# Optimization experiments

Measured on AMD Instinct MI355X. Metric: run time of the kernel, lower is better.

Reference implementation:

```python
import jax, jax.numpy as jnp
import numpy as np
from jax import lax

B, T, IN, H = 256, 128, 512, 1024
C = IN + H  # concat size


def setup_inputs() -> dict:
    key = jax.random.key(0)
    ks = jax.random.split(key, 32)
    d = {}
    names = ["F", "O", "CY", "CI", "CP", "CN", "IY", "II", "IP", "IN"]
    for i, n in enumerate(names):
        d["W" + n] = jax.random.normal(ks[i], (C, H), jnp.float32) * (2.0 / C) ** 0.5
        d["b" + n] = jax.random.uniform(ks[10 + i], (H,), jnp.float32)
    d["wA"] = jax.random.normal(ks[20], (H, H), jnp.float32) * (2.0 / H) ** 0.5
    for j, n in enumerate(["bAY", "bAI", "bAP", "bAN"]):
        d[n] = jax.random.uniform(ks[21 + j], (H,), jnp.float32)
    for j, n in enumerate(["factorY", "factorI", "factorP", "factorN"]):
        d[n] = jax.random.normal(ks[25 + j], (B, T, IN), jnp.float32)
    return d


def reference(factorY, factorI, factorP, factorN,
              WF, bF, WO, bO, WCY, bCY, WCI, bCI, WCP, bCP, WCN, bCN,
              WIY, bIY, WII, bII, WIP, bIP, WIN, bIN,
              wA, bAY, bAI, bAP, bAN):
    Bq = factorY.shape[0]
    Hq = WF.shape[1]

    def step(carry, xs):
        cT, hT = carry
        yT, iT, pT, nT = xs
        hy = jnp.concatenate([hT, yT], -1)  # [B, C]
        hi = jnp.concatenate([hT, iT], -1)
        hp = jnp.concatenate([hT, pT], -1)
        hn = jnp.concatenate([hT, nT], -1)
        f = jax.nn.sigmoid(hy @ WF + bF)
        o = jax.nn.sigmoid(hy @ WO + bO)
        # candidate memories gated by input gates (all input gates use hTyT, per source)
        lY = jnp.tanh(hy @ WCY + bCY) * jax.nn.sigmoid(hy @ WIY + bIY)
        lI = jnp.tanh(hi @ WCI + bCI) * jax.nn.sigmoid(hy @ WII + bII)
        lP = jnp.tanh(hp @ WCP + bCP) * jax.nn.sigmoid(hy @ WIP + bIP)
        lN = jnp.tanh(hn @ WCN + bCN) * jax.nn.sigmoid(hy @ WIN + bIN)
        cwa = cT @ wA  # [B, H]
        # faithful quirk: [B,1] score + [H] bias broadcasts to [B,H]; softmax over 4H
        att = jnp.concatenate([
            jnp.tanh(jnp.sum(lY * cwa, -1, keepdims=True) + bAY),
            jnp.tanh(jnp.sum(lI * cwa, -1, keepdims=True) + bAI),
            jnp.tanh(jnp.sum(lP * cwa, -1, keepdims=True) + bAP),
            jnp.tanh(jnp.sum(lN * cwa, -1, keepdims=True) + bAN)], -1)  # [B, 4H]
        a = jax.nn.softmax(att, -1)
        lT = a[:, 0:1] * lY + a[:, 1:2] * lI + a[:, 2:3] * lP + a[:, 3:4] * lN
        cN = cT * f + lT
        hN = jnp.tanh(cN) * o
        return (cN, hN), hN

    xs = (jnp.swapaxes(factorY, 0, 1), jnp.swapaxes(factorI, 0, 1),
          jnp.swapaxes(factorP, 0, 1), jnp.swapaxes(factorN, 0, 1))
    z = jnp.zeros((Bq, Hq), factorY.dtype)
    _, hs = lax.scan(step, (z, z), xs)  # hs: [T, B, H]
    return jnp.swapaxes(hs, 0, 1)  # [B, T, H]
```

## Files before the change

kernel.cpp:

```cpp
#include <hip/hip_runtime.h>
#include <hip/hip_bf16.h>

#define H_ 1024
#define C_ 1536
#define B_ 256
#define T_ 128
#define IN_ 512
#define BH_ (B_*H_)

typedef __hip_bfloat16 bf16;
typedef __attribute__((ext_vector_type(8))) short short8;
typedef __attribute__((ext_vector_type(4))) float f32x4;
typedef unsigned int u32;

struct WPtrs { const float* W[10]; const float* wA; };
struct BPtrs { const float* b[10]; const float* bA[4]; };

__device__ __forceinline__ float sigmf(float x){ return 1.0f/(1.0f + __expf(-x)); }
__device__ __forceinline__ float tanhfast(float x){ return 1.0f - 2.0f/(__expf(2.0f*x) + 1.0f); }

__device__ __forceinline__ ushort bf16bits(float f){
    bf16 b = __float2bfloat16(f);
    return *reinterpret_cast<ushort*>(&b);
}
__device__ __forceinline__ float bf2f(ushort u){
    bf16 b = *reinterpret_cast<bf16*>(&u);
    return __bfloat162float(b);
}

__device__ __forceinline__ void gload16(const void* g, void* l){
    __builtin_amdgcn_global_load_lds((const __attribute__((address_space(1))) u32*)g,
                                     (__attribute__((address_space(3))) u32*)l, 16, 0, 0);
}

__global__ void transpose_w(WPtrs wp, ushort* __restrict__ Wt, ushort* __restrict__ wAt)
{
    int g = blockIdx.z;
    int K = (g==10) ? H_ : C_;
    int k0 = blockIdx.x*32, n0 = blockIdx.y*32;
    if (k0 >= K) return;
    const float* src = (g==10) ? wp.wA : wp.W[g];
    __shared__ float tile[32][33];
    int tx = threadIdx.x, ty = threadIdx.y;
    #pragma unroll
    for (int i=0;i<32;i+=8)
        tile[ty+i][tx] = src[(size_t)(k0+ty+i)*H_ + n0 + tx];
    __syncthreads();
    ushort* dst = (g==10) ? wAt : (Wt + (size_t)g*H_*C_);
    #pragma unroll
    for (int i=0;i<32;i+=8)
        dst[(size_t)(n0+ty+i)*K + k0 + tx] = bf16bits(tile[tx][ty+i]);
}

__global__ void convert_x(const float* __restrict__ xY, const float* __restrict__ xI,
                          const float* __restrict__ xP, const float* __restrict__ xN,
                          ushort* __restrict__ xb)
{
    size_t idx = (size_t)blockIdx.x*blockDim.x + threadIdx.x;
    size_t base = idx*4;
    size_t a = base >> 24;
    size_t off = base & ((size_t)(1u<<24)-1);
    const float* s = (a==0)?xY:(a==1)?xI:(a==2)?xP:xN;
    float4 v = *(const float4*)(s + off);
    ushort4 o;
    o.x = bf16bits(v.x); o.y = bf16bits(v.y); o.z = bf16bits(v.z); o.w = bf16bits(v.w);
    *(ushort4*)(xb + base) = o;
}

__global__ __launch_bounds__(256) void xp_gemm(const ushort* __restrict__ Wt,
                                               const ushort* __restrict__ xb,
                                               ushort* __restrict__ Xp)
{
    int bid = blockIdx.x;
    int xcd = bid & 7, lid = bid >> 3;
    int ntile = xcd*20 + (lid >> 9);
    int mtile = lid & 511;
    int g = ntile >> 4;
    int n0g = (ntile & 15)*64;
    int tq = mtile >> 2;
    int b0 = (mtile & 3)*64;
    int xs = (g==3)?1:(g==4)?2:(g==5)?3:0;
    const ushort* xsrc = xb + (size_t)xs*((size_t)B_*T_*IN_);
    const ushort* Bbase = Wt + (size_t)g*H_*C_ + 1024;

    __shared__ ushort As[64][64];
    __shared__ ushort Bs[64][64];
    int tid = threadIdx.x;
    int wid = tid>>6, lane = tid&63;
    int wr = wid>>1, wc = wid&1;

    f32x4 acc[2][2] = {};
    for (int k0=0; k0<IN_; k0+=64){
        #pragma unroll
        for (int it=0; it<2; ++it){
            int cid = it*256 + tid;
            int row = cid>>3, kc = cid&7;
            int kcs = kc ^ (row&7);
            gload16(xsrc + ((size_t)(b0+row)*T_ + tq)*IN_ + k0 + kcs*8,
                    (ushort*)As + (size_t)(it*256 + wid*64)*8);
        }
        #pragma unroll
        for (int it=0; it<2; ++it){
            int cid = it*256 + tid;
            int row = cid>>3, kc = cid&7;
            int kcs = kc ^ (row&7);
            gload16(Bbase + (size_t)(n0g+row)*C_ + k0 + kcs*8,
                    (ushort*)Bs + (size_t)(it*256 + wid*64)*8);
        }
        __syncthreads();
        #pragma unroll
        for (int kk=0; kk<2; ++kk){
            short8 af[2], bfr[2];
            #pragma unroll
            for (int mr=0;mr<2;++mr){
                int r = wr*32 + mr*16 + (lane&15);
                int j = (kk*4 + (lane>>4)) ^ (r&7);
                af[mr] = *(const short8*)((ushort*)As + r*64 + j*8);
            }
            #pragma unroll
            for (int nr=0;nr<2;++nr){
                int r = wc*32 + nr*16 + (lane&15);
                int j = (kk*4 + (lane>>4)) ^ (r&7);
                bfr[nr] = *(const short8*)((ushort*)Bs + r*64 + j*8);
            }
            #pragma unroll
            for (int mr=0;mr<2;++mr)
                #pragma unroll
                for (int nr=0;nr<2;++nr)
                    acc[mr][nr] = __builtin_amdgcn_mfma_f32_16x16x32_bf16(af[mr], bfr[nr], acc[mr][nr], 0,0,0);
        }
        __syncthreads();
    }
    ushort* Xg = Xp + (((size_t)tq*10 + g)*B_ + b0)*H_ + n0g;
    #pragma unroll
    for (int mr=0;mr<2;++mr){
        #pragma unroll
        for (int nr=0;nr<2;++nr){
            int col = wc*32 + nr*16 + (lane&15);
            #pragma unroll
            for (int r=0;r<4;++r){
                int row = wr*32 + mr*16 + (lane>>4)*4 + r;
                Xg[(size_t)row*H_ + col] = bf16bits(acc[mr][nr][r]);
            }
        }
    }
}

template<bool XP>
__global__ __launch_bounds__(256) void gemm_step(
    const ushort* __restrict__ Wt, const ushort* __restrict__ wAt,
    const ushort* __restrict__ xb, const ushort* __restrict__ hb,
    const ushort* __restrict__ cbuf, const ushort* __restrict__ Xp,
    float* __restrict__ P, int t)
{
    int bid = blockIdx.x;
    int xcd = bid & 7, lid = bid >> 3;
    int ntile = xcd*22 + (lid >> 2);
    int mtile = lid & 3;
    int nglob0 = ntile*64;
    int g = nglob0 >> 10;
    int n0g = nglob0 & 1023;
    int m0 = mtile*64;
    bool isA = (g==10);
    const ushort* Bbase = isA ? wAt : (Wt + (size_t)g*H_*C_);
    size_t Bstride = isA ? 1024 : 1536;
    int K = XP ? 1024 : (isA ? 1024 : 1536);
    int xs = (g==3)?1:(g==4)?2:(g==5)?3:0;
    const ushort* xsrc = xb + (size_t)xs*((size_t)B_*T_*IN_);
    const ushort* Ah = isA ? cbuf : hb;

    __shared__ ushort As[64][64];
    __shared__ ushort Bs[64][64];
    int tid = threadIdx.x;
    int wid = tid>>6, lane = tid&63;
    int wr = wid>>1, wc = wid&1;

    f32x4 acc[2][2] = {};
    if (XP && !isA){
        const ushort* Xg = Xp + (((size_t)t*10 + g)*B_ + m0)*H_ + n0g;
        #pragma unroll
        for (int mr=0;mr<2;++mr)
            #pragma unroll
            for (int nr=0;nr<2;++nr){
                int col = wc*32 + nr*16 + (lane&15);
                #pragma unroll
                for (int r=0;r<4;++r){
                    int row = wr*32 + mr*16 + (lane>>4)*4 + r;
                    acc[mr][nr][r] = bf2f(Xg[(size_t)row*H_ + col]);
                }
            }
    }

    for (int k0=0; k0<K; k0+=64){
        #pragma unroll
        for (int it=0; it<2; ++it){
            int cid = it*256 + tid;
            int row = cid>>3, kc = cid&7;
            int kcs = kc ^ (row&7);
            int k = k0 + kcs*8;
            const ushort* src;
            if (XP || isA || k < 1024) src = Ah + (size_t)(m0+row)*H_ + k;
            else                       src = xsrc + ((size_t)(m0+row)*T_ + t)*IN_ + (k-1024);
            gload16(src, (ushort*)As + (size_t)(it*256 + wid*64)*8);
        }
        #pragma unroll
        for (int it=0; it<2; ++it){
            int cid = it*256 + tid;
            int row = cid>>3, kc = cid&7;
            int kcs = kc ^ (row&7);
            gload16(Bbase + (size_t)(n0g+row)*Bstride + k0 + kcs*8,
                    (ushort*)Bs + (size_t)(it*256 + wid*64)*8);
        }
        __syncthreads();
        #pragma unroll
        for (int kk=0; kk<2; ++kk){
            short8 af[2], bfr[2];
            #pragma unroll
            for (int mr=0;mr<2;++mr){
                int r = wr*32 + mr*16 + (lane&15);
                int j = (kk*4 + (lane>>4)) ^ (r&7);
                af[mr] = *(const short8*)((ushort*)As + r*64 + j*8);
            }
            #pragma unroll
            for (int nr=0;nr<2;++nr){
                int r = wc*32 + nr*16 + (lane&15);
                int j = (kk*4 + (lane>>4)) ^ (r&7);
                bfr[nr] = *(const short8*)((ushort*)Bs + r*64 + j*8);
            }
            #pragma unroll
            for (int mr=0;mr<2;++mr)
                #pragma unroll
                for (int nr=0;nr<2;++nr)
                    acc[mr][nr] = __builtin_amdgcn_mfma_f32_16x16x32_bf16(af[mr], bfr[nr], acc[mr][nr], 0,0,0);
        }
        __syncthreads();
    }
    float* Pg = P + (size_t)g*BH_;
    #pragma unroll
    for (int mr=0;mr<2;++mr){
        #pragma unroll
        for (int nr=0;nr<2;++nr){
            int col = n0g + wc*32 + nr*16 + (lane&15);
            #pragma unroll
            for (int r=0;r<4;++r){
                int rowg = m0 + wr*32 + mr*16 + (lane>>4)*4 + r;
                Pg[(size_t)rowg*H_ + col] = acc[mr][nr][r];
            }
        }
    }
}

__global__ __launch_bounds__(256) void step_update(
    const float* __restrict__ P, BPtrs bp,
    float* __restrict__ c, ushort* __restrict__ hb, ushort* __restrict__ cbuf,
    float* __restrict__ out, int t)
{
    int b = blockIdx.x;
    int tid = threadIdx.x;
    int wid = tid>>6, lane = tid&63;
    const float* Pb = P + (size_t)b*H_;

    float lY[4], lI[4], lPv[4], lN[4], fv[4], ov[4], cw[4];
    #pragma unroll
    for (int q=0;q<4;++q){
        int j = tid + q*256;
        fv[q] = sigmf(Pb[(size_t)0*BH_ + j] + bp.b[0][j]);
        ov[q] = sigmf(Pb[(size_t)1*BH_ + j] + bp.b[1][j]);
        lY[q]  = tanhfast(Pb[(size_t)2*BH_ + j] + bp.b[2][j]) * sigmf(Pb[(size_t)6*BH_ + j] + bp.b[6][j]);
        lI[q]  = tanhfast(Pb[(size_t)3*BH_ + j] + bp.b[3][j]) * sigmf(Pb[(size_t)7*BH_ + j] + bp.b[7][j]);
        lPv[q] = tanhfast(Pb[(size_t)4*BH_ + j] + bp.b[4][j]) * sigmf(Pb[(size_t)8*BH_ + j] + bp.b[8][j]);
        lN[q]  = tanhfast(Pb[(size_t)5*BH_ + j] + bp.b[5][j]) * sigmf(Pb[(size_t)9*BH_ + j] + bp.b[9][j]);
        cw[q] = Pb[(size_t)10*BH_ + j];
    }
    float v0=0,v1=0,v2=0,v3=0;
    #pragma unroll
    for (int q=0;q<4;++q){
        v0 += lY[q]*cw[q]; v1 += lI[q]*cw[q]; v2 += lPv[q]*cw[q]; v3 += lN[q]*cw[q];
    }
    #pragma unroll
    for (int d=32; d>=1; d>>=1){
        v0 += __shfl_down(v0,d); v1 += __shfl_down(v1,d);
        v2 += __shfl_down(v2,d); v3 += __shfl_down(v3,d);
    }
    __shared__ float red[4][4];
    if (lane==0){ red[wid][0]=v0; red[wid][1]=v1; red[wid][2]=v2; red[wid][3]=v3; }
    __syncthreads();
    float sY = red[0][0]+red[1][0]+red[2][0]+red[3][0];
    float sI = red[0][1]+red[1][1]+red[2][1]+red[3][1];
    float sP = red[0][2]+red[1][2]+red[2][2]+red[3][2];
    float sN = red[0][3]+red[1][3]+red[2][3]+red[3][3];

    float zp = 0.f;
    #pragma unroll
    for (int q=0;q<4;++q){
        int j = tid + q*256;
        zp += __expf(tanhfast(sY + bp.bA[0][j]));
        zp += __expf(tanhfast(sI + bp.bA[1][j]));
        zp += __expf(tanhfast(sP + bp.bA[2][j]));
        zp += __expf(tanhfast(sN + bp.bA[3][j]));
    }
    #pragma unroll
    for (int d=32; d>=1; d>>=1) zp += __shfl_down(zp,d);
    __shared__ float zred[4];
    if (lane==0) zred[wid] = zp;
    __syncthreads();
    float Z = zred[0]+zred[1]+zred[2]+zred[3];
    float Zi = 1.0f / Z;
    float a0 = __expf(tanhfast(sY + bp.bA[0][0]))*Zi;
    float a1 = __expf(tanhfast(sY + bp.bA[0][1]))*Zi;
    float a2 = __expf(tanhfast(sY + bp.bA[0][2]))*Zi;
    float a3 = __expf(tanhfast(sY + bp.bA[0][3]))*Zi;

    #pragma unroll
    for (int q=0;q<4;++q){
        int j = tid + q*256;
        float lT = a0*lY[q] + a1*lI[q] + a2*lPv[q] + a3*lN[q];
        float cn = c[(size_t)b*H_ + j]*fv[q] + lT;
        c[(size_t)b*H_ + j] = cn;
        cbuf[(size_t)b*H_ + j] = bf16bits(cn);
        float hn = tanhfast(cn)*ov[q];
        hb[(size_t)b*H_ + j] = bf16bits(hn);
        out[((size_t)b*T_ + t)*H_ + j] = hn;
    }
}

extern "C" void kernel_launch(void* const* d_in, const int* in_sizes, int n_in,
                              void* d_out, int out_size, void* d_ws, size_t ws_size,
                              hipStream_t stream)
{
    WPtrs wp; BPtrs bp;
    for (int i=0;i<10;++i){ wp.W[i] = (const float*)d_in[2*i]; bp.b[i] = (const float*)d_in[2*i+1]; }
    wp.wA = (const float*)d_in[20];
    for (int i=0;i<4;++i) bp.bA[i] = (const float*)d_in[21+i];
    const float* xY = (const float*)d_in[25];
    const float* xI = (const float*)d_in[26];
    const float* xP = (const float*)d_in[27];
    const float* xN = (const float*)d_in[28];

    char* w = (char*)d_ws;
    size_t off = 0;
    ushort* Wt  = (ushort*)(w+off); off += (size_t)10*H_*C_*2;
    ushort* wAt = (ushort*)(w+off); off += (size_t)H_*H_*2;
    ushort* xb  = (ushort*)(w+off); off += (size_t)4*B_*T_*IN_*2;
    float*  P   = (float*)(w+off);  off += (size_t)11*BH_*4;
    float*  c   = (float*)(w+off);  off += (size_t)BH_*4;
    ushort* hb  = (ushort*)(w+off); off += (size_t)BH_*2;
    ushort* cbuf= (ushort*)(w+off); off += (size_t)BH_*2;
    ushort* Xp  = (ushort*)(w+off);
    size_t need_xp = off + (size_t)T_*10*B_*H_*2;
    bool xp_ok = (ws_size >= need_xp);

    hipMemsetAsync(c, 0, (size_t)BH_*8, stream);

    transpose_w<<<dim3(C_/32, H_/32, 11), dim3(32,8), 0, stream>>>(wp, Wt, wAt);
    convert_x<<<(4u*B_*T_*IN_/4)/256, 256, 0, stream>>>(xY,xI,xP,xN, xb);

    float* out = (float*)d_out;
    if (xp_ok){
        xp_gemm<<<81920, 256, 0, stream>>>(Wt, xb, Xp);
        for (int t=0;t<T_;++t){
            gemm_step<true><<<704, 256, 0, stream>>>(Wt, wAt, xb, hb, cbuf, Xp, P, t);
            step_update<<<B_, 256, 0, stream>>>(P, bp, c, hb, cbuf, out, t);
        }
    } else {
        for (int t=0;t<T_;++t){
            gemm_step<false><<<704, 256, 0, stream>>>(Wt, wAt, xb, hb, cbuf, Xp, P, t);
            step_update<<<B_, 256, 0, stream>>>(P, bp, c, hb, cbuf, out, t);
        }
    }
}
```

Baseline: 3.814 ms.

## Double-buffer LDS tiles in step GEMM and widen step_update to 1024 threads

The per-step GEMM now keeps two LDS buffers for the A and B tiles. The next K-slice is issued before the current slice's MFMAs run, and one barrier per iteration replaces two, so global loads can overlap compute. The Xp accumulator preload now comes after the first stage is issued. The step_update kernel uses 1024 threads with one element each instead of 256 threads with four, adjusting the reductions to 16 waves. This doubles LDS use per block, which may reduce occupancy, and larger blocks change how work is scheduled across CUs.

```diff
diff --git a/kernel.cpp b/kernel.cpp
--- a/kernel.cpp
+++ b/kernel.cpp
@@ -169,29 +169,15 @@
     const ushort* xsrc = xb + (size_t)xs*((size_t)B_*T_*IN_);
     const ushort* Ah = isA ? cbuf : hb;
 
-    __shared__ ushort As[64][64];
-    __shared__ ushort Bs[64][64];
+    __shared__ ushort As[2][64*64];
+    __shared__ ushort Bs[2][64*64];
     int tid = threadIdx.x;
     int wid = tid>>6, lane = tid&63;
     int wr = wid>>1, wc = wid&1;
 
-    f32x4 acc[2][2] = {};
-    if (XP && !isA){
-        const ushort* Xg = Xp + (((size_t)t*10 + g)*B_ + m0)*H_ + n0g;
-        #pragma unroll
-        for (int mr=0;mr<2;++mr)
-            #pragma unroll
-            for (int nr=0;nr<2;++nr){
-                int col = wc*32 + nr*16 + (lane&15);
-                #pragma unroll
-                for (int r=0;r<4;++r){
-                    int row = wr*32 + mr*16 + (lane>>4)*4 + r;
-                    acc[mr][nr][r] = bf2f(Xg[(size_t)row*H_ + col]);
-                }
-            }
-    }
-
-    for (int k0=0; k0<K; k0+=64){
+    auto stage = [&](int buf, int k0){
+        ushort* la = As[buf];
+        ushort* lb = Bs[buf];
         #pragma unroll
         for (int it=0; it<2; ++it){
             int cid = it*256 + tid;
@@ -201,7 +187,7 @@
             const ushort* src;
             if (XP || isA || k < 1024) src = Ah + (size_t)(m0+row)*H_ + k;
             else                       src = xsrc + ((size_t)(m0+row)*T_ + t)*IN_ + (k-1024);
-            gload16(src, (ushort*)As + (size_t)(it*256 + wid*64)*8);
+            gload16(src, la + (size_t)(it*256 + wid*64)*8);
         }
         #pragma unroll
         for (int it=0; it<2; ++it){
@@ -209,9 +195,35 @@
             int row = cid>>3, kc = cid&7;
             int kcs = kc ^ (row&7);
             gload16(Bbase + (size_t)(n0g+row)*Bstride + k0 + kcs*8,
-                    (ushort*)Bs + (size_t)(it*256 + wid*64)*8);
-        }
-        __syncthreads();
+                    lb + (size_t)(it*256 + wid*64)*8);
+        }
+    };
+
+    f32x4 acc[2][2] = {};
+    stage(0, 0);
+
+    if (XP && !isA){
+        const ushort* Xg = Xp + (((size_t)t*10 + g)*B_ + m0)*H_ + n0g;
+        #pragma unroll
+        for (int mr=0;mr<2;++mr)
+            #pragma unroll
+            for (int nr=0;nr<2;++nr){
+                int col = wc*32 + nr*16 + (lane&15);
+                #pragma unroll
+                for (int r=0;r<4;++r){
+                    int row = wr*32 + mr*16 + (lane>>4)*4 + r;
+                    acc[mr][nr][r] = bf2f(Xg[(size_t)row*H_ + col]);
+                }
+            }
+    }
+    __syncthreads();
+
+    int nIter = K >> 6;
+    for (int i=0; i<nIter; ++i){
+        int cur = i & 1;
+        if (i+1 < nIter) stage(cur^1, (i+1)<<6);
+        ushort* la = As[cur];
+        ushort* lb = Bs[cur];
         #pragma unroll
         for (int kk=0; kk<2; ++kk){
             short8 af[2], bfr[2];
@@ -219,13 +231,13 @@
             for (int mr=0;mr<2;++mr){
                 int r = wr*32 + mr*16 + (lane&15);
                 int j = (kk*4 + (lane>>4)) ^ (r&7);
-                af[mr] = *(const short8*)((ushort*)As + r*64 + j*8);
+                af[mr] = *(const short8*)(la + r*64 + j*8);
             }
             #pragma unroll
             for (int nr=0;nr<2;++nr){
                 int r = wc*32 + nr*16 + (lane&15);
                 int j = (kk*4 + (lane>>4)) ^ (r&7);
-                bfr[nr] = *(const short8*)((ushort*)Bs + r*64 + j*8);
+                bfr[nr] = *(const short8*)(lb + r*64 + j*8);
             }
             #pragma unroll
             for (int mr=0;mr<2;++mr)
@@ -235,6 +247,7 @@
         }
         __syncthreads();
     }
+
     float* Pg = P + (size_t)g*BH_;
     #pragma unroll
     for (int mr=0;mr<2;++mr){
@@ -250,78 +263,64 @@
     }
 }
 
-__global__ __launch_bounds__(256) void step_update(
+__global__ __launch_bounds__(1024) void step_update(
     const float* __restrict__ P, BPtrs bp,
     float* __restrict__ c, ushort* __restrict__ hb, ushort* __restrict__ cbuf,
     float* __restrict__ out, int t)
 {
     int b = blockIdx.x;
-    int tid = threadIdx.x;
-    int wid = tid>>6, lane = tid&63;
+    int j = threadIdx.x;
+    int wid = j>>6, lane = j&63;
     const float* Pb = P + (size_t)b*H_;
 
-    float lY[4], lI[4], lPv[4], lN[4], fv[4], ov[4], cw[4];
-    #pragma unroll
-    for (int q=0;q<4;++q){
-        int j = tid + q*256;
-        fv[q] = sigmf(Pb[(size_t)0*BH_ + j] + bp.b[0][j]);
-        ov[q] = sigmf(Pb[(size_t)1*BH_ + j] + bp.b[1][j]);
-        lY[q]  = tanhfast(Pb[(size_t)2*BH_ + j] + bp.b[2][j]) * sigmf(Pb[(size_t)6*BH_ + j] + bp.b[6][j]);
-        lI[q]  = tanhfast(Pb[(size_t)3*BH_ + j] + bp.b[3][j]) * sigmf(Pb[(size_t)7*BH_ + j] + bp.b[7][j]);
-        lPv[q] = tanhfast(Pb[(size_t)4*BH_ + j] + bp.b[4][j]) * sigmf(Pb[(size_t)8*BH_ + j] + bp.b[8][j]);
-        lN[q]  = tanhfast(Pb[(size_t)5*BH_ + j] + bp.b[5][j]) * sigmf(Pb[(size_t)9*BH_ + j] + bp.b[9][j]);
-        cw[q] = Pb[(size_t)10*BH_ + j];
-    }
-    float v0=0,v1=0,v2=0,v3=0;
-    #pragma unroll
-    for (int q=0;q<4;++q){
-        v0 += lY[q]*cw[q]; v1 += lI[q]*cw[q]; v2 += lPv[q]*cw[q]; v3 += lN[q]*cw[q];
-    }
+    float fv = sigmf(Pb[(size_t)0*BH_ + j] + bp.b[0][j]);
+    float ov = sigmf(Pb[(size_t)1*BH_ + j] + bp.b[1][j]);
+    float lY = tanhfast(Pb[(size_t)2*BH_ + j] + bp.b[2][j]) * sigmf(Pb[(size_t)6*BH_ + j] + bp.b[6][j]);
+    float lI = tanhfast(Pb[(size_t)3*BH_ + j] + bp.b[3][j]) * sigmf(Pb[(size_t)7*BH_ + j] + bp.b[7][j]);
+    float lP = tanhfast(Pb[(size_t)4*BH_ + j] + bp.b[4][j]) * sigmf(Pb[(size_t)8*BH_ + j] + bp.b[8][j]);
+    float lN = tanhfast(Pb[(size_t)5*BH_ + j] + bp.b[5][j]) * sigmf(Pb[(size_t)9*BH_ + j] + bp.b[9][j]);
+    float cw = Pb[(size_t)10*BH_ + j];
+
+    float v0=lY*cw, v1=lI*cw, v2=lP*cw, v3=lN*cw;
     #pragma unroll
     for (int d=32; d>=1; d>>=1){
         v0 += __shfl_down(v0,d); v1 += __shfl_down(v1,d);
         v2 += __shfl_down(v2,d); v3 += __shfl_down(v3,d);
     }
-    __shared__ float red[4][4];
+    __shared__ float red[16][4];
     if (lane==0){ red[wid][0]=v0; red[wid][1]=v1; red[wid][2]=v2; red[wid][3]=v3; }
     __syncthreads();
-    float sY = red[0][0]+red[1][0]+red[2][0]+red[3][0];
-    float sI = red[0][1]+red[1][1]+red[2][1]+red[3][1];
-    float sP = red[0][2]+red[1][2]+red[2][2]+red[3][2];
-    float sN = red[0][3]+red[1][3]+red[2][3]+red[3][3];
-
-    float zp = 0.f;
-    #pragma unroll
-    for (int q=0;q<4;++q){
-        int j = tid + q*256;
-        zp += __expf(tanhfast(sY + bp.bA[0][j]));
-        zp += __expf(tanhfast(sI + bp.bA[1][j]));
-        zp += __expf(tanhfast(sP + bp.bA[2][j]));
-        zp += __expf(tanhfast(sN + bp.bA[3][j]));
-    }
+    float sY=0, sI=0, sP=0, sN=0;
+    #pragma unroll
+    for (int w=0; w<16; ++w){
+        sY += red[w][0]; sI += red[w][1]; sP += red[w][2]; sN += red[w][3];
+    }
+
+    float zp = __expf(tanhfast(sY + bp.bA[0][j]))
+             + __expf(tanhfast(sI + bp.bA[1][j]))
+             + __expf(tanhfast(sP + bp.bA[2][j]))
+             + __expf(tanhfast(sN + bp.bA[3][j]));
     #pragma unroll
     for (int d=32; d>=1; d>>=1) zp += __shfl_down(zp,d);
-    __shared__ float zred[4];
+    __shared__ float zred[16];
     if (lane==0) zred[wid] = zp;
     __syncthreads();
-    float Z = zred[0]+zred[1]+zred[2]+zred[3];
+    float Z = 0;
+    #pragma unroll
+    for (int w=0; w<16; ++w) Z += zred[w];
     float Zi = 1.0f / Z;
     float a0 = __expf(tanhfast(sY + bp.bA[0][0]))*Zi;
     float a1 = __expf(tanhfast(sY + bp.bA[0][1]))*Zi;
     float a2 = __expf(tanhfast(sY + bp.bA[0][2]))*Zi;
     float a3 = __expf(tanhfast(sY + bp.bA[0][3]))*Zi;
 
-    #pragma unroll
-    for (int q=0;q<4;++q){
-        int j = tid + q*256;
-        float lT = a0*lY[q] + a1*lI[q] + a2*lPv[q] + a3*lN[q];
-        float cn = c[(size_t)b*H_ + j]*fv[q] + lT;
-        c[(size_t)b*H_ + j] = cn;
-        cbuf[(size_t)b*H_ + j] = bf16bits(cn);
-        float hn = tanhfast(cn)*ov[q];
-        hb[(size_t)b*H_ + j] = bf16bits(hn);
-        out[((size_t)b*T_ + t)*H_ + j] = hn;
-    }
+    float lT = a0*lY + a1*lI + a2*lP + a3*lN;
+    float cn = c[(size_t)b*H_ + j]*fv + lT;
+    c[(size_t)b*H_ + j] = cn;
+    cbuf[(size_t)b*H_ + j] = bf16bits(cn);
+    float hn = tanhfast(cn)*ov;
+    hb[(size_t)b*H_ + j] = bf16bits(hn);
+    out[((size_t)b*T_ + t)*H_ + j] = hn;
 }
 
 extern "C" void kernel_launch(void* const* d_in, const int* in_sizes, int n_in,
@@ -360,12 +359,12 @@
         xp_gemm<<<81920, 256, 0, stream>>>(Wt, xb, Xp);
         for (int t=0;t<T_;++t){
             gemm_step<true><<<704, 256, 0, stream>>>(Wt, wAt, xb, hb, cbuf, Xp, P, t);
-            step_update<<<B_, 256, 0, stream>>>(P, bp, c, hb, cbuf, out, t);
+            step_update<<<B_, 1024, 0, stream>>>(P, bp, c, hb, cbuf, out, t);
         }
     } else {
         for (int t=0;t<T_;++t){
             gemm_step<false><<<704, 256, 0, stream>>>(Wt, wAt, xb, hb, cbuf, Xp, P, t);
-            step_update<<<B_, 256, 0, stream>>>(P, bp, c, hb, cbuf, out, t);
-        }
-    }
-}
+            step_update<<<B_, 1024, 0, stream>>>(P, bp, c, hb, cbuf, out, t);
+        }
+    }
+}
```

After: 3.676 ms. -3.6%, faster.
